# Kernel tuning notes

Hardware: AMD Instinct MI355X
Metric: run time of the kernel (lower is better)

## Reference

```python
import jax, jax.numpy as jnp
import numpy as np

N = 100_000      # nodes
E = 1_600_000    # edges (avg degree 16)
D = 128          # emb_dim == hidden_dim
OUT = 128        # out_dim
NUM_BOND_TYPE = 6
NUM_BOND_DIR = 3


def _xavier(key, fan_in, fan_out, shape):
    a = np.sqrt(6.0 / (fan_in + fan_out)).astype(np.float32)
    return jax.random.uniform(key, shape, jnp.float32, -a, a)


def setup_inputs() -> dict:
    key = jax.random.key(0)
    ks = jax.random.split(key, 12)
    x = jax.random.normal(ks[0], (N, D), jnp.float32)
    edge_index = jax.random.randint(ks[1], (2, E), 0, N)
    edge_attr = jax.random.randint(ks[2], (E, 2), 0, NUM_BOND_DIR)
    # PReLU single learnable slope (torch init 0.25)
    prelu_a = jnp.full((1,), 0.25, jnp.float32)
    # enc_to_dec: Linear(D, D, bias=False), torch default uniform(-1/sqrt(D), 1/sqrt(D))
    s = 1.0 / np.sqrt(D)
    W_enc = jax.random.uniform(ks[3], (D, D), jnp.float32, -s, s)
    # edge embedding tables, xavier_uniform
    emb1 = _xavier(ks[4], NUM_BOND_TYPE, D, (NUM_BOND_TYPE, D))
    emb2 = _xavier(ks[5], NUM_BOND_DIR, D, (NUM_BOND_DIR, D))
    # GIN MLP: Linear(D, 2D) -> ReLU -> Linear(2D, OUT)
    W1 = jax.random.uniform(ks[6], (2 * D, D), jnp.float32, -s, s)
    b1 = jax.random.uniform(ks[7], (2 * D,), jnp.float32, -s, s)
    s2 = 1.0 / np.sqrt(2 * D)
    W2 = jax.random.uniform(ks[8], (OUT, 2 * D), jnp.float32, -s2, s2)
    b2 = jax.random.uniform(ks[9], (OUT,), jnp.float32, -s2, s2)
    return {
        "x": x, "edge_index": edge_index, "edge_attr": edge_attr,
        "prelu_a": prelu_a, "W_enc": W_enc,
        "emb1": emb1, "emb2": emb2,
        "W1": W1, "b1": b1, "W2": W2, "b2": b2,
    }


def reference(x, edge_index, edge_attr, prelu_a, W_enc, emb1, emb2, W1, b1, W2, b2):
    # PReLU then enc_to_dec (no bias)
    h = jnp.where(x >= 0, x, prelu_a * x)          # [N, D]
    h = h @ W_enc.T                                 # [N, D]
    src, dst = edge_index[0], edge_index[1]
    # edge embeddings for real edges
    e_emb = emb1[edge_attr[:, 0]] + emb2[edge_attr[:, 1]]  # [E, D]
    # messages: x_j + edge_attr, scatter-add at dst
    msg = h[src] + e_emb                             # [E, D]
    agg = jax.ops.segment_sum(msg, dst, num_segments=N)    # [N, D]
    # self-loops: appended edge (i, i) with attr [4, 0]
    self_emb = emb1[4] + emb2[0]                     # [D]
    agg = agg + h + self_emb[None, :]
    # GIN update MLP
    hid = jax.nn.relu(agg @ W1.T + b1)               # [N, 2D]
    out = hid @ W2.T + b2                            # [N, OUT]
    return out
```

## Files before the change

### kernel.cpp

```cpp
#include <hip/hip_runtime.h>
#include <hip/hip_bf16.h>

#define DD 128

typedef short bf16x8 __attribute__((ext_vector_type(8)));
typedef float f32x4 __attribute__((ext_vector_type(4)));

__device__ __forceinline__ float bf2f_lo(unsigned int u) {
    union { unsigned int v; float f; } x; x.v = u << 16; return x.f;
}
__device__ __forceinline__ float bf2f_hi(unsigned int u) {
    union { unsigned int v; float f; } x; x.v = u & 0xFFFF0000u; return x.f;
}
__device__ __forceinline__ unsigned short f2bf(float f) {
    union { float f; unsigned int u; } x; x.f = f;
    unsigned int u = x.u;
    unsigned int r = (u + 0x7FFFu + ((u >> 16) & 1u)) >> 16;
    return (unsigned short)r;
}

#define SBSH 7
#define SBN  128
#define NBP  256
#define NSBMAX 800
#define PKCAP 4096

__global__ __launch_bounds__(256) void sbwc_k(
    const int* __restrict__ ei, int* __restrict__ bh,
    const float* __restrict__ Wenc, const float* __restrict__ W1,
    const float* __restrict__ W2, unsigned short* __restrict__ wb,
    int E, int chunk, int nsb)
{
    __shared__ int h4[4][NSBMAX];
    const int b = blockIdx.x;
    if (b < NBP) {
        int wid = threadIdx.x >> 6;
        for (int i = threadIdx.x; i < 4 * NSBMAX; i += 256) ((int*)h4)[i] = 0;
        __syncthreads();
        int beg = b * chunk, end = min(E, beg + chunk);
        for (int e = beg + threadIdx.x; e < end; e += 256)
            atomicAdd(&h4[wid][ei[E + e] >> SBSH], 1);
        __syncthreads();
        for (int i = threadIdx.x; i < nsb; i += 256)
            bh[i * NBP + b] = h4[0][i] + h4[1][i] + h4[2][i] + h4[3][i];
        return;
    }
    int i = ((b - NBP) * 256 + threadIdx.x) * 4;
    if (i >= 81920) return;
    const float* src;
    int off;
    if (i < 16384)      { src = Wenc; off = 0; }
    else if (i < 49152) { src = W1;   off = 16384; }
    else                { src = W2;   off = 49152; }
    float4 v = *(const float4*)&src[i - off];
    ushort4 w;
    w.x = f2bf(v.x); w.y = f2bf(v.y); w.z = f2bf(v.z); w.w = f2bf(v.w);
    *(ushort4*)&wb[i] = w;
}

__global__ __launch_bounds__(256) void pscan1_k(const int* __restrict__ bh,
                                                int* __restrict__ bsum, int ntot) {
    __shared__ int ws[4];
    int base = blockIdx.x * 2048 + threadIdx.x * 8;
    int s = 0;
    #pragma unroll
    for (int i = 0; i < 8; ++i) { int idx = base + i; if (idx < ntot) s += bh[idx]; }
    int lane = threadIdx.x & 63, wid = threadIdx.x >> 6;
    int ss = s;
    #pragma unroll
    for (int o = 1; o < 64; o <<= 1) { int t = __shfl_up(ss, o, 64); if (lane >= o) ss += t; }
    if (lane == 63) ws[wid] = ss;
    __syncthreads();
    if (threadIdx.x == 0) bsum[blockIdx.x] = ws[0] + ws[1] + ws[2] + ws[3];
}

__global__ __launch_bounds__(256) void pscan3_k(const int* __restrict__ bh,
                                                const int* __restrict__ bsum,
                                                int* __restrict__ bho, int ntot) {
    __shared__ int ws[4];
    __shared__ int boff;
    const int b = blockIdx.x;
    const int t = threadIdx.x;
    const int lane = t & 63, wid = t >> 6;

    int pv = (t < b) ? bsum[t] : 0;
    #pragma unroll
    for (int o = 32; o; o >>= 1) pv += __shfl_xor(pv, o, 64);
    if (lane == 0) ws[wid] = pv;
    __syncthreads();
    if (t == 0) boff = ws[0] + ws[1] + ws[2] + ws[3];
    __syncthreads();

    int base = b * 2048 + t * 8;
    int v[8]; int s = 0;
    #pragma unroll
    for (int i = 0; i < 8; ++i) { int idx = base + i; v[i] = (idx < ntot) ? bh[idx] : 0; s += v[i]; }
    int ss = s;
    #pragma unroll
    for (int o = 1; o < 64; o <<= 1) { int u = __shfl_up(ss, o, 64); if (lane >= o) ss += u; }
    if (lane == 63) ws[wid] = ss;
    __syncthreads();
    if (t == 0) { int c = 0; for (int w = 0; w < 4; ++w) { int u = ws[w]; ws[w] = c; c += u; } }
    __syncthreads();
    int excl = ss - s + ws[wid] + boff;
    #pragma unroll
    for (int i = 0; i < 8; ++i) {
        int idx = base + i;
        if (idx < ntot) bho[idx] = excl;
        excl += v[i];
    }
}

__global__ __launch_bounds__(256) void pg_k(
    const int* __restrict__ ei, const int* __restrict__ ea,
    const int* __restrict__ bho, int* __restrict__ rec,
    const float* __restrict__ x, const unsigned short* __restrict__ Wb,
    unsigned short* __restrict__ Hb, const float* __restrict__ prelu_a,
    int E, int chunk, int nsb, int M)
{
    __shared__ int cur[NSBMAX];
    const int tid = threadIdx.x;

    if (blockIdx.x < NBP) {
        int b = blockIdx.x;
        for (int i = tid; i < nsb; i += 256) cur[i] = bho[i * NBP + b];
        __syncthreads();
        int beg = b * chunk, end = min(E, beg + chunk);
        for (int e = beg + tid; e < end; e += 256) {
            int src = ei[e];
            int dst = ei[E + e];
            int2 aa = *(const int2*)&ea[2 * e];
            int pos = atomicAdd(&cur[dst >> SBSH], 1);
            rec[pos] = src | ((aa.x * 3 + aa.y) << 17) | ((dst & (SBN - 1)) << 21);
        }
        return;
    }

    const int K = 128;
    const int wid = tid >> 6, lane = tid & 63;
    const float pa = prelu_a[0];
    const int r0 = (blockIdx.x - NBP) * 128 + wid * 32;
    const int rl = lane & 15, kb = (lane >> 4) * 8;

    bf16x8 af[2][4];
    #pragma unroll
    for (int rf = 0; rf < 2; ++rf) {
        int row = r0 + rf * 16 + rl; if (row > M - 1) row = M - 1;
        #pragma unroll
        for (int kf = 0; kf < 4; ++kf) {
            float4 v0 = *(const float4*)&x[(size_t)row * K + kf * 32 + kb];
            float4 v1 = *(const float4*)&x[(size_t)row * K + kf * 32 + kb + 4];
            v0.x = v0.x >= 0.f ? v0.x : pa * v0.x;
            v0.y = v0.y >= 0.f ? v0.y : pa * v0.y;
            v0.z = v0.z >= 0.f ? v0.z : pa * v0.z;
            v0.w = v0.w >= 0.f ? v0.w : pa * v0.w;
            v1.x = v1.x >= 0.f ? v1.x : pa * v1.x;
            v1.y = v1.y >= 0.f ? v1.y : pa * v1.y;
            v1.z = v1.z >= 0.f ? v1.z : pa * v1.z;
            v1.w = v1.w >= 0.f ? v1.w : pa * v1.w;
            bf16x8 t;
            t[0] = (short)f2bf(v0.x); t[1] = (short)f2bf(v0.y);
            t[2] = (short)f2bf(v0.z); t[3] = (short)f2bf(v0.w);
            t[4] = (short)f2bf(v1.x); t[5] = (short)f2bf(v1.y);
            t[6] = (short)f2bf(v1.z); t[7] = (short)f2bf(v1.w);
            af[rf][kf] = t;
        }
    }

    f32x4 acc[8][2];
    const f32x4 zz = {0.f, 0.f, 0.f, 0.f};
    #pragma unroll
    for (int nt = 0; nt < 8; ++nt) { acc[nt][0] = zz; acc[nt][1] = zz; }

    #pragma unroll
    for (int nt = 0; nt < 8; ++nt) {
        bf16x8 bf[4];
        #pragma unroll
        for (int kf = 0; kf < 4; ++kf)
            bf[kf] = *(const bf16x8*)&Wb[(size_t)(nt * 16 + rl) * K + kf * 32 + kb];
        #pragma unroll
        for (int rf = 0; rf < 2; ++rf)
            #pragma unroll
            for (int kf = 0; kf < 4; ++kf)
                acc[nt][rf] = __builtin_amdgcn_mfma_f32_16x16x32_bf16(af[rf][kf], bf[kf], acc[nt][rf], 0, 0, 0);
    }

    const int rq = (lane >> 4) * 4;
    #pragma unroll
    for (int nt = 0; nt < 8; ++nt) {
        int c = nt * 16 + rl;
        #pragma unroll
        for (int rf = 0; rf < 2; ++rf) {
            int rb = r0 + rf * 16 + rq;
            #pragma unroll
            for (int t = 0; t < 4; ++t) {
                int r = rb + t;
                if (r < M) Hb[(size_t)r * 128 + c] = f2bf(acc[nt][rf][t]);
            }
        }
    }
}

__global__ __launch_bounds__(1024) void cam_k(
    const unsigned short* __restrict__ h,
    const int* __restrict__ rec,
    const int* __restrict__ bho,
    const float* __restrict__ emb1, const float* __restrict__ emb2,
    int* __restrict__ packed,
    const unsigned short* __restrict__ w1b, const float* __restrict__ b1,
    const unsigned short* __restrict__ w2b, const float* __restrict__ b2,
    float* __restrict__ out,
    int nsb, int M, int E)
{
    __shared__ float emb12[10][DD];
    __shared__ int hist[SBN];
    __shared__ int lstart[SBN];
    __shared__ int wsum[2];
    __shared__ unsigned short W1l[256][136];
    __shared__ char U[67584];
    int* pkl = (int*)U;
    unsigned short (*aggl)[136] = (unsigned short (*)[136])(U + 16384);
    unsigned short (*hidl)[264] = (unsigned short (*)[264])U;
    unsigned short (*W2l)[264] = (unsigned short (*)[264])&W1l[0][0];

    const int s = blockIdx.x;
    const int t = threadIdx.x;
    const int lane = t & 63, wid = t >> 6;
    const int rl = lane & 15, kb = (lane >> 4) * 8;
    const int rq = (lane >> 4) * 4;

    for (int idx = t; idx < 256 * 16; idx += 1024) {
        int n = idx >> 4, kq = idx & 15;
        *(ushort4*)&W1l[n][kq * 8] = *(const ushort4*)&w1b[(size_t)n * 128 + kq * 8];
        *(ushort4*)&W1l[n][kq * 8 + 4] = *(const ushort4*)&w1b[(size_t)n * 128 + kq * 8 + 4];
    }
    for (int i = t; i < 10 * DD; i += 1024) {
        int c = i >> 7, col = i & 127;
        float v;
        if (c == 9) v = emb1[4 * DD + col] + emb2[col];
        else        v = emb1[(c / 3) * DD + col] + emb2[(c % 3) * DD + col];
        emb12[c][col] = v;
    }
    int sb0 = bho[s * NBP];
    int sb1 = (s == nsb - 1) ? E : bho[(s + 1) * NBP];
    if (t < SBN) hist[t] = 0;
    __syncthreads();

    const bool inlds = (sb1 - sb0) <= PKCAP;

    for (int i = sb0 + t; i < sb1; i += 1024)
        atomicAdd(&hist[(rec[i] >> 21) & (SBN - 1)], 1);
    __syncthreads();

    int v = (t < SBN) ? hist[t] : 0;
    int ss = v;
    #pragma unroll
    for (int o = 1; o < 64; o <<= 1) { int u = __shfl_up(ss, o, 64); if (lane >= o) ss += u; }
    if (t < SBN && lane == 63) wsum[wid] = ss;
    __syncthreads();
    if (t == 0) { int c = 0; for (int w = 0; w < 2; ++w) { int x2 = wsum[w]; wsum[w] = c; c += x2; } }
    __syncthreads();
    if (t < SBN) {
        lstart[t] = ss - v + wsum[wid];
        hist[t] = 0;
    }
    __syncthreads();

    if (inlds) {
        for (int i = sb0 + t; i < sb1; i += 1024) {
            int r = rec[i];
            int dl = (r >> 21) & (SBN - 1);
            int pos = lstart[dl] + atomicAdd(&hist[dl], 1);
            pkl[pos] = r & 0x1FFFFF;
        }
    } else {
        for (int i = sb0 + t; i < sb1; i += 1024) {
            int r = rec[i];
            int dl = (r >> 21) & (SBN - 1);
            int pos = sb0 + lstart[dl] + atomicAdd(&hist[dl], 1);
            packed[pos] = r & 0x1FFFFF;
        }
    }
    __syncthreads();

    const int n0 = s << SBSH;
    const int c2 = lane * 2;
    #pragma unroll
    for (int k = 0; k < SBN / 16; ++k) {
        int r = wid + k * 16;
        int n = n0 + r;
        if (n >= M) continue;
        int lbeg = lstart[r];
        int lend = lbeg + hist[r];
        unsigned int hn = *(const unsigned int*)&h[(size_t)n * DD + c2];
        float2 acc = {bf2f_lo(hn) + emb12[9][c2], bf2f_hi(hn) + emb12[9][c2 + 1]};
        if (inlds) {
            int e = lbeg;
            for (; e + 8 <= lend; e += 8) {
                int p[8]; unsigned int hv[8]; float2 m[8];
                #pragma unroll
                for (int i = 0; i < 8; ++i) p[i] = pkl[e + i];
                #pragma unroll
                for (int i = 0; i < 8; ++i)
                    hv[i] = *(const unsigned int*)&h[(size_t)(p[i] & 0x1FFFF) * DD + c2];
                #pragma unroll
                for (int i = 0; i < 8; ++i)
                    m[i] = *(const float2*)&emb12[(p[i] >> 17) & 15][c2];
                #pragma unroll
                for (int i = 0; i < 8; ++i) {
                    acc.x += bf2f_lo(hv[i]) + m[i].x;
                    acc.y += bf2f_hi(hv[i]) + m[i].y;
                }
            }
            for (; e < lend; ++e) {
                int p = pkl[e];
                unsigned int hv = *(const unsigned int*)&h[(size_t)(p & 0x1FFFF) * DD + c2];
                float2 m = *(const float2*)&emb12[(p >> 17) & 15][c2];
                acc.x += bf2f_lo(hv) + m.x;
                acc.y += bf2f_hi(hv) + m.y;
            }
        } else {
            int e = sb0 + lbeg, end = sb0 + lend;
            for (; e + 8 <= end; e += 8) {
                int p[8]; unsigned int hv[8]; float2 m[8];
                #pragma unroll
                for (int i = 0; i < 8; ++i) p[i] = packed[e + i];
                #pragma unroll
                for (int i = 0; i < 8; ++i)
                    hv[i] = *(const unsigned int*)&h[(size_t)(p[i] & 0x1FFFF) * DD + c2];
                #pragma unroll
                for (int i = 0; i < 8; ++i)
                    m[i] = *(const float2*)&emb12[(p[i] >> 17) & 15][c2];
                #pragma unroll
                for (int i = 0; i < 8; ++i) {
                    acc.x += bf2f_lo(hv[i]) + m[i].x;
                    acc.y += bf2f_hi(hv[i]) + m[i].y;
                }
            }
            for (; e < end; ++e) {
                int p = packed[e];
                unsigned int hv = *(const unsigned int*)&h[(size_t)(p & 0x1FFFF) * DD + c2];
                float2 m = *(const float2*)&emb12[(p >> 17) & 15][c2];
                acc.x += bf2f_lo(hv) + m.x;
                acc.y += bf2f_hi(hv) + m.y;
            }
        }
        *(unsigned int*)&aggl[r][c2] = ((unsigned int)f2bf(acc.y) << 16) | f2bf(acc.x);
    }
    __syncthreads();

    const int rf = wid & 7, ch = wid >> 3;
    bf16x8 af[4];
    #pragma unroll
    for (int kf = 0; kf < 4; ++kf)
        af[kf] = *(const bf16x8*)&aggl[rf * 16 + rl][kf * 32 + kb];
    __syncthreads();

    f32x4 acc1[8];
    const f32x4 zz = {0.f, 0.f, 0.f, 0.f};
    #pragma unroll
    for (int j = 0; j < 8; ++j) acc1[j] = zz;
    #pragma unroll
    for (int j = 0; j < 8; ++j) {
        int nt = ch * 8 + j;
        bf16x8 bf[4];
        #pragma unroll
        for (int kf = 0; kf < 4; ++kf)
            bf[kf] = *(const bf16x8*)&W1l[nt * 16 + rl][kf * 32 + kb];
        #pragma unroll
        for (int kf = 0; kf < 4; ++kf)
            acc1[j] = __builtin_amdgcn_mfma_f32_16x16x32_bf16(af[kf], bf[kf], acc1[j], 0, 0, 0);
    }
    #pragma unroll
    for (int j = 0; j < 8; ++j) {
        int c = (ch * 8 + j) * 16 + rl;
        float bi = b1[c];
        #pragma unroll
        for (int tt = 0; tt < 4; ++tt)
            hidl[rf * 16 + rq + tt][c] = f2bf(fmaxf(acc1[j][tt] + bi, 0.f));
    }
    __syncthreads();

    for (int idx = t; idx < 128 * 32; idx += 1024) {
        int n = idx >> 5, kq = idx & 31;
        *(ushort4*)&W2l[n][kq * 8] = *(const ushort4*)&w2b[(size_t)n * 256 + kq * 8];
        *(ushort4*)&W2l[n][kq * 8 + 4] = *(const ushort4*)&w2b[(size_t)n * 256 + kq * 8 + 4];
    }
    bf16x8 af2[8];
    #pragma unroll
    for (int kf = 0; kf < 8; ++kf)
        af2[kf] = *(const bf16x8*)&hidl[rf * 16 + rl][kf * 32 + kb];
    __syncthreads();

    f32x4 acc2[4];
    #pragma unroll
    for (int j = 0; j < 4; ++j) acc2[j] = zz;
    #pragma unroll
    for (int j = 0; j < 4; ++j) {
        int nt = ch * 4 + j;
        bf16x8 bf[8];
        #pragma unroll
        for (int kf = 0; kf < 8; ++kf)
            bf[kf] = *(const bf16x8*)&W2l[nt * 16 + rl][kf * 32 + kb];
        #pragma unroll
        for (int kf = 0; kf < 8; ++kf)
            acc2[j] = __builtin_amdgcn_mfma_f32_16x16x32_bf16(af2[kf], bf[kf], acc2[j], 0, 0, 0);
    }
    #pragma unroll
    for (int j = 0; j < 4; ++j) {
        int c = (ch * 4 + j) * 16 + rl;
        float bi = b2[c];
        #pragma unroll
        for (int tt = 0; tt < 4; ++tt) {
            int r = n0 + rf * 16 + rq + tt;
            if (r < M) out[(size_t)r * 128 + c] = acc2[j][tt] + bi;
        }
    }
}

extern "C" void kernel_launch(void* const* d_in, const int* in_sizes, int n_in,
                              void* d_out, int out_size, void* d_ws, size_t ws_size,
                              hipStream_t stream) {
    const float* x     = (const float*)d_in[0];
    const int*   ei    = (const int*)d_in[1];
    const int*   ea    = (const int*)d_in[2];
    const float* pa    = (const float*)d_in[3];
    const float* Wenc  = (const float*)d_in[4];
    const float* emb1  = (const float*)d_in[5];
    const float* emb2  = (const float*)d_in[6];
    const float* W1    = (const float*)d_in[7];
    const float* b1    = (const float*)d_in[8];
    const float* W2    = (const float*)d_in[9];
    const float* b2    = (const float*)d_in[10];
    float* out = (float*)d_out;

    const int M = in_sizes[0] / DD;
    const int E = in_sizes[1] / 2;
    const int nsb = (M + SBN - 1) >> SBSH;
    const int chunk = (E + NBP - 1) / NBP;
    const int ntot = nsb * NBP;
    const int nscb = (ntot + 2047) / 2048;

    char* ws = (char*)d_ws;
    size_t o = 0;
    unsigned short* h_bf  = (unsigned short*)(ws + o); o += (size_t)M * DD * 2;
    int* rec    = (int*)(ws + o); o += (size_t)E * 4;
    int* packed = (int*)(ws + o); o += (size_t)E * 4;
    int* bh     = (int*)(ws + o); o += (size_t)ntot * 4;
    int* bho    = (int*)(ws + o); o += (size_t)ntot * 4;
    int* bsum   = (int*)(ws + o); o += (size_t)nscb * 4;
    unsigned short* wb = (unsigned short*)(ws + o); o += 81920 * 2;
    unsigned short* wenc_b = wb;
    unsigned short* w1_b   = wb + 16384;
    unsigned short* w2_b   = wb + 49152;

    const int gm = (M + 127) / 128;
    dim3 blk(256);

    sbwc_k<<<dim3(NBP + 80), blk, 0, stream>>>(ei, bh, Wenc, W1, W2, wb, E, chunk, nsb);

    pscan1_k<<<dim3(nscb), blk, 0, stream>>>(bh, bsum, ntot);
    pscan3_k<<<dim3(nscb), blk, 0, stream>>>(bh, bsum, bho, ntot);

    pg_k<<<dim3(NBP + gm), blk, 0, stream>>>(
        ei, ea, bho, rec, x, wenc_b, h_bf, pa, E, chunk, nsb, M);

    cam_k<<<dim3(nsb), dim3(1024), 0, stream>>>(
        h_bf, rec, bho, emb1, emb2, packed,
        w1_b, b1, w2_b, b2, out, nsb, M, E);
}
```

Measured before the change: 204.6 us.

## Split fused aggregation+MLP kernel into separate aggregation and MLP kernels

```diff
diff --git a/kernel.cpp b/kernel.cpp
--- a/kernel.cpp
+++ b/kernel.cpp
@@ -201,39 +201,23 @@
     }
 }
 
-__global__ __launch_bounds__(1024) void cam_k(
+__global__ __launch_bounds__(1024) void csragg_k(
     const unsigned short* __restrict__ h,
     const int* __restrict__ rec,
     const int* __restrict__ bho,
     const float* __restrict__ emb1, const float* __restrict__ emb2,
-    int* __restrict__ packed,
-    const unsigned short* __restrict__ w1b, const float* __restrict__ b1,
-    const unsigned short* __restrict__ w2b, const float* __restrict__ b2,
-    float* __restrict__ out,
+    int* __restrict__ packed, unsigned int* __restrict__ aggb,
     int nsb, int M, int E)
 {
     __shared__ float emb12[10][DD];
     __shared__ int hist[SBN];
     __shared__ int lstart[SBN];
     __shared__ int wsum[2];
-    __shared__ unsigned short W1l[256][136];
-    __shared__ char U[67584];
-    int* pkl = (int*)U;
-    unsigned short (*aggl)[136] = (unsigned short (*)[136])(U + 16384);
-    unsigned short (*hidl)[264] = (unsigned short (*)[264])U;
-    unsigned short (*W2l)[264] = (unsigned short (*)[264])&W1l[0][0];
-
+    __shared__ int pkl[PKCAP];
     const int s = blockIdx.x;
     const int t = threadIdx.x;
     const int lane = t & 63, wid = t >> 6;
-    const int rl = lane & 15, kb = (lane >> 4) * 8;
-    const int rq = (lane >> 4) * 4;
-
-    for (int idx = t; idx < 256 * 16; idx += 1024) {
-        int n = idx >> 4, kq = idx & 15;
-        *(ushort4*)&W1l[n][kq * 8] = *(const ushort4*)&w1b[(size_t)n * 128 + kq * 8];
-        *(ushort4*)&W1l[n][kq * 8 + 4] = *(const ushort4*)&w1b[(size_t)n * 128 + kq * 8 + 4];
-    }
+
     for (int i = t; i < 10 * DD; i += 1024) {
         int c = i >> 7, col = i & 127;
         float v;
@@ -345,15 +329,41 @@
                 acc.y += bf2f_hi(hv) + m.y;
             }
         }
-        *(unsigned int*)&aggl[r][c2] = ((unsigned int)f2bf(acc.y) << 16) | f2bf(acc.x);
-    }
-    __syncthreads();
-
+        aggb[((size_t)n * DD + c2) >> 1] = ((unsigned int)f2bf(acc.y) << 16) | f2bf(acc.x);
+    }
+}
+
+__global__ __launch_bounds__(1024) void mlp_k(
+    const unsigned short* __restrict__ A,
+    const unsigned short* __restrict__ w1b,
+    const float* __restrict__ b1,
+    const unsigned short* __restrict__ w2b,
+    const float* __restrict__ b2,
+    float* __restrict__ out, int M)
+{
+    __shared__ unsigned short W1l[256][136];
+    __shared__ unsigned short hidl[128][264];
+    unsigned short (*W2l)[264] = (unsigned short (*)[264])&W1l[0][0];
+
+    const int tid = threadIdx.x;
+    const int wid = tid >> 6, lane = tid & 63;
+    const int rl = lane & 15, kb = (lane >> 4) * 8;
+    const int rq = (lane >> 4) * 4;
     const int rf = wid & 7, ch = wid >> 3;
+    const int r0 = blockIdx.x * 128;
+
+    for (int idx = tid; idx < 256 * 16; idx += 1024) {
+        int n = idx >> 4, kq = idx & 15;
+        *(ushort4*)&W1l[n][kq * 8] = *(const ushort4*)&w1b[(size_t)n * 128 + kq * 8];
+        *(ushort4*)&W1l[n][kq * 8 + 4] = *(const ushort4*)&w1b[(size_t)n * 128 + kq * 8 + 4];
+    }
     bf16x8 af[4];
-    #pragma unroll
-    for (int kf = 0; kf < 4; ++kf)
-        af[kf] = *(const bf16x8*)&aggl[rf * 16 + rl][kf * 32 + kb];
+    {
+        int row = r0 + rf * 16 + rl; if (row > M - 1) row = M - 1;
+        #pragma unroll
+        for (int kf = 0; kf < 4; ++kf)
+            af[kf] = *(const bf16x8*)&A[(size_t)row * 128 + kf * 32 + kb];
+    }
     __syncthreads();
 
     f32x4 acc1[8];
@@ -381,7 +391,7 @@
     }
     __syncthreads();
 
-    for (int idx = t; idx < 128 * 32; idx += 1024) {
+    for (int idx = tid; idx < 128 * 32; idx += 1024) {
         int n = idx >> 5, kq = idx & 31;
         *(ushort4*)&W2l[n][kq * 8] = *(const ushort4*)&w2b[(size_t)n * 256 + kq * 8];
         *(ushort4*)&W2l[n][kq * 8 + 4] = *(const ushort4*)&w2b[(size_t)n * 256 + kq * 8 + 4];
@@ -412,7 +422,7 @@
         float bi = b2[c];
         #pragma unroll
         for (int tt = 0; tt < 4; ++tt) {
-            int r = n0 + rf * 16 + rq + tt;
+            int r = r0 + rf * 16 + rq + tt;
             if (r < M) out[(size_t)r * 128 + c] = acc2[j][tt] + bi;
         }
     }
@@ -444,6 +454,7 @@
     char* ws = (char*)d_ws;
     size_t o = 0;
     unsigned short* h_bf  = (unsigned short*)(ws + o); o += (size_t)M * DD * 2;
+    unsigned int*   aggb  = (unsigned int*)(ws + o);   o += (size_t)M * DD * 2;
     int* rec    = (int*)(ws + o); o += (size_t)E * 4;
     int* packed = (int*)(ws + o); o += (size_t)E * 4;
     int* bh     = (int*)(ws + o); o += (size_t)ntot * 4;
@@ -465,7 +476,9 @@
     pg_k<<<dim3(NBP + gm), blk, 0, stream>>>(
         ei, ea, bho, rec, x, wenc_b, h_bf, pa, E, chunk, nsb, M);
 
-    cam_k<<<dim3(nsb), dim3(1024), 0, stream>>>(
-        h_bf, rec, bho, emb1, emb2, packed,
-        w1_b, b1, w2_b, b2, out, nsb, M, E);
-}
+    csragg_k<<<dim3(nsb), dim3(1024), 0, stream>>>(
+        h_bf, rec, bho, emb1, emb2, packed, aggb, nsb, M, E);
+
+    mlp_k<<<dim3(gm), dim3(1024), 0, stream>>>(
+        (const unsigned short*)aggb, w1_b, b1, w2_b, b2, out, M);
+}
```

New measurement: 182.9 us (median of 2 runs). -10.6%, faster.
